# Performance work log

Measured on AMD Instinct MI355X. Metric: run time of the kernel, lower is better.

The kernel has to match this reference:

```python
import jax, jax.numpy as jnp
import numpy as np

B, D, M = 16384, 256, 262144

def setup_inputs() -> dict:
    key = jax.random.key(0)
    k1, k2, k3 = jax.random.split(key, 3)
    return {
        "features": jax.random.normal(k1, (B, D), dtype=jnp.float32),
        "attention_quality": jax.random.uniform(k2, (), dtype=jnp.float32),
        "memory_attentions": jax.random.normal(k3, (M, D), dtype=jnp.float32),
        "memory_utilities": jnp.ones((M,), dtype=jnp.float32),
        "memory_index": 1000,  # Python int (static circular-buffer start)
    }

def reference(features, attention_quality, memory_attentions, memory_utilities, memory_index):
    b, d = features.shape
    m = memory_attentions.shape[0]
    # circular-buffer write positions: (memory_index + i) % m, i = 0..b-1
    idx = (memory_index + jnp.arange(b)) % m  # static since memory_index is a Python int
    new_mem = memory_attentions.at[idx].set(features)
    new_util = memory_utilities.at[idx].set(attention_quality)
    new_index = (memory_index + b) % m          # Python int
    full = (memory_index + b) >= m              # Python bool (initial memory_full=False)
    utilization = jnp.asarray(1.0 if full else new_index / m, dtype=jnp.float32)
    quality = new_util[:new_index].mean()       # static slice
    return new_mem, new_util, utilization, quality
```

## Files before the change

### kernel.cpp

```cpp
#include <hip/hip_runtime.h>

constexpr int B  = 16384;
constexpr int D  = 256;
constexpr int M  = 262144;
constexpr int D4 = D / 4;
constexpr int LOG_D4 = 6;

typedef float f32x4 __attribute__((ext_vector_type(4)));

constexpr int THREADS    = 256;
constexpr int MEM_BLOCKS = 2048;
constexpr int TOTAL4     = M * D4;
constexpr int STRIDE     = MEM_BLOCKS * THREADS;
constexpr int ROWSTRIDE  = STRIDE >> LOG_D4;
constexpr int ITERS      = TOTAL4 / STRIDE;
constexpr int BATCH      = 8;

constexpr int UTIL_BLOCKS = 256;

__global__ __launch_bounds__(THREADS) void fused_kernel(
    const f32x4* __restrict__ mem,
    const f32x4* __restrict__ feat,
    const f32x4* __restrict__ util,
    const float* __restrict__ aq_p,
    const int*   __restrict__ mi_p,
    f32x4*       __restrict__ out_mem,
    f32x4*       __restrict__ out_util,
    float*       __restrict__ block_sums)
{
    const int s = ((*mi_p) % M + M) % M;

    if (blockIdx.x < UTIL_BLOCKS) {
        const int   mi   = *mi_p;
        const int   nidx = (mi + B) % M;
        const float aq   = *aq_p;
        const int   i4   = blockIdx.x * THREADS + threadIdx.x;
        const f32x4 u    = util[i4];
        f32x4 o;
        float local = 0.f;
        const int base = i4 * 4;
#pragma unroll
        for (int j = 0; j < 4; ++j) {
            const int i = base + j;
            int rel = i - s;
            if (rel < 0) rel += M;
            const float v = (rel < B) ? aq : u[j];
            o[j] = v;
            if (i < nidx) local += v;
        }
        out_util[i4] = o;

        for (int off = 32; off > 0; off >>= 1)
            local += __shfl_down(local, off, 64);
        __shared__ float wsum[THREADS / 64];
        const int lane = threadIdx.x & 63;
        const int wid  = threadIdx.x >> 6;
        if (lane == 0) wsum[wid] = local;
        __syncthreads();
        if (threadIdx.x == 0) {
            float s2 = 0.f;
#pragma unroll
            for (int w = 0; w < THREADS / 64; ++w) s2 += wsum[w];
            block_sums[blockIdx.x] = s2;
        }
    }

    const int tid  = blockIdx.x * THREADS + threadIdx.x;
    const int col  = tid & (D4 - 1);
    const int row0 = tid >> LOG_D4;
#pragma unroll
    for (int ib = 0; ib < ITERS / BATCH; ++ib) {
        f32x4 vals[BATCH];
#pragma unroll
        for (int j = 0; j < BATCH; ++j) {
            const int it  = ib * BATCH + j;
            const int row = row0 + it * ROWSTRIDE;
            int rel = row - s;
            if (rel < 0) rel += M;
            if (rel < B) {
                vals[j] = feat[(rel << LOG_D4) | col];
            } else {
                vals[j] = mem[tid + it * STRIDE];
            }
        }
#pragma unroll
        for (int j = 0; j < BATCH; ++j) {
            const int it = ib * BATCH + j;
            __builtin_nontemporal_store(vals[j], &out_mem[tid + it * STRIDE]);
        }
    }
}

__global__ __launch_bounds__(256) void finalize_kernel(
    const float* __restrict__ block_sums,
    const int*   __restrict__ mi_p,
    float*       __restrict__ out_scalars)
{
    const int  mi   = *mi_p;
    const int  nidx = (mi + B) % M;
    const bool full = (mi + B) >= M;

    float v = (threadIdx.x < UTIL_BLOCKS) ? block_sums[threadIdx.x] : 0.f;
    for (int off = 32; off > 0; off >>= 1)
        v += __shfl_down(v, off, 64);
    __shared__ float wsum[4];
    if ((threadIdx.x & 63) == 0) wsum[threadIdx.x >> 6] = v;
    __syncthreads();
    if (threadIdx.x == 0) {
        const float sum = wsum[0] + wsum[1] + wsum[2] + wsum[3];
        out_scalars[0] = full ? 1.0f : (float)nidx / (float)M;
        out_scalars[1] = sum / (float)nidx;
    }
}

extern "C" void kernel_launch(void* const* d_in, const int* in_sizes, int n_in,
                              void* d_out, int out_size, void* d_ws, size_t ws_size,
                              hipStream_t stream)
{
    const float* feat = (const float*)d_in[0];
    const float* aq   = (const float*)d_in[1];
    const float* mem  = (const float*)d_in[2];
    const float* util = (const float*)d_in[3];
    const int*   mi   = (const int*)  d_in[4];

    float* out         = (float*)d_out;
    float* out_mem     = out;
    float* out_util    = out + (size_t)M * D;
    float* out_scalars = out_util + M;
    float* block_sums  = (float*)d_ws;

    fused_kernel<<<MEM_BLOCKS, THREADS, 0, stream>>>(
        (const f32x4*)mem, (const f32x4*)feat, (const f32x4*)util,
        aq, mi, (f32x4*)out_mem, (f32x4*)out_util, block_sums);

    finalize_kernel<<<1, 256, 0, stream>>>(block_sums, mi, out_scalars);
}
```

Baseline: 96.44 us.

## Compute quality scalar in-kernel analytically and drop finalize kernel launch

Replaces the two-pass reduction over the written utility buffer and the separate finalize kernel with a closed-form quality computed by the last block. That block sums only the untouched prefix of the input utilities and adds B times the written quality. This removes a second kernel launch and its dependency, and also makes the utility output store non-temporal. The risk is that the last block does a serial prefix sum of up to s elements, and the full-buffer case uses different logic than before.

```diff
diff --git a/kernel.cpp b/kernel.cpp
--- a/kernel.cpp
+++ b/kernel.cpp
@@ -21,47 +21,57 @@
 __global__ __launch_bounds__(THREADS) void fused_kernel(
     const f32x4* __restrict__ mem,
     const f32x4* __restrict__ feat,
-    const f32x4* __restrict__ util,
+    const f32x4* __restrict__ util4,
+    const float* __restrict__ utilf,
     const float* __restrict__ aq_p,
     const int*   __restrict__ mi_p,
     f32x4*       __restrict__ out_mem,
     f32x4*       __restrict__ out_util,
-    float*       __restrict__ block_sums)
+    float*       __restrict__ out_scalars)
 {
     const int s = ((*mi_p) % M + M) % M;
 
     if (blockIdx.x < UTIL_BLOCKS) {
-        const int   mi   = *mi_p;
-        const int   nidx = (mi + B) % M;
-        const float aq   = *aq_p;
-        const int   i4   = blockIdx.x * THREADS + threadIdx.x;
-        const f32x4 u    = util[i4];
+        const float aq = *aq_p;
+        const int   i4 = blockIdx.x * THREADS + threadIdx.x;
+        const f32x4 u  = util4[i4];
         f32x4 o;
-        float local = 0.f;
         const int base = i4 * 4;
 #pragma unroll
         for (int j = 0; j < 4; ++j) {
             const int i = base + j;
             int rel = i - s;
             if (rel < 0) rel += M;
-            const float v = (rel < B) ? aq : u[j];
-            o[j] = v;
-            if (i < nidx) local += v;
+            o[j] = (rel < B) ? aq : u[j];
         }
-        out_util[i4] = o;
+        __builtin_nontemporal_store(o, &out_util[i4]);
+    } else if (blockIdx.x == MEM_BLOCKS - 1) {
+        const float aq   = *aq_p;
+        const int   nidx = (s + B) % M;
+        const bool  full = (s + B) >= M;
 
+        float local = 0.f;
+        if (!full) {
+            for (int i = threadIdx.x; i < s; i += THREADS)
+                local += utilf[i];
+        }
         for (int off = 32; off > 0; off >>= 1)
             local += __shfl_down(local, off, 64);
         __shared__ float wsum[THREADS / 64];
-        const int lane = threadIdx.x & 63;
-        const int wid  = threadIdx.x >> 6;
-        if (lane == 0) wsum[wid] = local;
+        if ((threadIdx.x & 63) == 0) wsum[threadIdx.x >> 6] = local;
         __syncthreads();
         if (threadIdx.x == 0) {
-            float s2 = 0.f;
+            float ssum = 0.f;
 #pragma unroll
-            for (int w = 0; w < THREADS / 64; ++w) s2 += wsum[w];
-            block_sums[blockIdx.x] = s2;
+            for (int w = 0; w < THREADS / 64; ++w) ssum += wsum[w];
+            float q;
+            if (full) {
+                q = (nidx > 0) ? aq : (0.0f / 0.0f);
+            } else {
+                q = (ssum + (float)B * aq) / (float)(s + B);
+            }
+            out_scalars[0] = full ? 1.0f : (float)nidx / (float)M;
+            out_scalars[1] = q;
         }
     }
 
@@ -91,28 +101,6 @@
     }
 }
 
-__global__ __launch_bounds__(256) void finalize_kernel(
-    const float* __restrict__ block_sums,
-    const int*   __restrict__ mi_p,
-    float*       __restrict__ out_scalars)
-{
-    const int  mi   = *mi_p;
-    const int  nidx = (mi + B) % M;
-    const bool full = (mi + B) >= M;
-
-    float v = (threadIdx.x < UTIL_BLOCKS) ? block_sums[threadIdx.x] : 0.f;
-    for (int off = 32; off > 0; off >>= 1)
-        v += __shfl_down(v, off, 64);
-    __shared__ float wsum[4];
-    if ((threadIdx.x & 63) == 0) wsum[threadIdx.x >> 6] = v;
-    __syncthreads();
-    if (threadIdx.x == 0) {
-        const float sum = wsum[0] + wsum[1] + wsum[2] + wsum[3];
-        out_scalars[0] = full ? 1.0f : (float)nidx / (float)M;
-        out_scalars[1] = sum / (float)nidx;
-    }
-}
-
 extern "C" void kernel_launch(void* const* d_in, const int* in_sizes, int n_in,
                               void* d_out, int out_size, void* d_ws, size_t ws_size,
                               hipStream_t stream)
@@ -127,11 +115,8 @@
     float* out_mem     = out;
     float* out_util    = out + (size_t)M * D;
     float* out_scalars = out_util + M;
-    float* block_sums  = (float*)d_ws;
 
     fused_kernel<<<MEM_BLOCKS, THREADS, 0, stream>>>(
-        (const f32x4*)mem, (const f32x4*)feat, (const f32x4*)util,
-        aq, mi, (f32x4*)out_mem, (f32x4*)out_util, block_sums);
-
-    finalize_kernel<<<1, 256, 0, stream>>>(block_sums, mi, out_scalars);
+        (const f32x4*)mem, (const f32x4*)feat, (const f32x4*)util, util,
+        aq, mi, (f32x4*)out_mem, (f32x4*)out_util, out_scalars);
 }
```

After: 89.93 us. 6.8% less time.
